# Performance work log

Hardware: AMD Instinct MI355X
Metric: run time of the kernel (lower is better)

The kernel has to match this reference:

```python
import jax, jax.numpy as jnp
import numpy as np

IN_DIM = 128
OUT_DIM = 128
NUM_RELS = 8
N_NODES = 50000
N_EDGES = 500000


def setup_inputs() -> dict:
    key = jax.random.key(0)
    k_x, k_ei_s, k_ei_d, k_et, k_w, k_sw = jax.random.split(key, 6)
    x = jax.random.normal(k_x, (N_NODES, IN_DIM), dtype=jnp.float32)
    src = jax.random.randint(k_ei_s, (N_EDGES,), 0, N_NODES)
    dst = jax.random.randint(k_ei_d, (N_EDGES,), 0, N_NODES)
    edge_index = jnp.stack([src, dst], axis=0).astype(jnp.int64)
    edge_type = jax.random.randint(k_et, (N_EDGES,), 0, NUM_RELS).astype(jnp.int64)
    # xavier_uniform: bound = sqrt(6/(fan_in+fan_out))
    bw = float(np.sqrt(6.0 / (IN_DIM + OUT_DIM)))
    weight = jax.random.uniform(k_w, (NUM_RELS, IN_DIM, OUT_DIM), dtype=jnp.float32, minval=-bw, maxval=bw)
    self_loop_weight = jax.random.uniform(k_sw, (IN_DIM, OUT_DIM), dtype=jnp.float32, minval=-bw, maxval=bw)
    bias = jnp.zeros((OUT_DIM,), dtype=jnp.float32)
    return {
        "x": x,
        "weight": weight,
        "self_loop_weight": self_loop_weight,
        "bias": bias,
        "edge_index": edge_index,
        "edge_type": edge_type,
        "num_entities": N_NODES,
    }


def reference(x, weight, self_loop_weight, bias, edge_index, edge_type, num_entities):
    # Relation-grouped formulation of the per-edge loop:
    # transform every node under every relation once: hr[r, n, o]
    hr = jnp.einsum("nd,rdo->rno", x, weight)
    src, dst = edge_index[0], edge_index[1]
    # per-edge message = x[src] @ weight[edge_type]  == hr[edge_type, src]
    msg = hr[edge_type, src]  # [E, out]
    agg = jax.ops.segment_sum(msg, dst, num_segments=num_entities)  # scatter-add into out[dst]
    out = agg + x @ self_loop_weight + bias
    return jax.nn.relu(out)
```

## Files before the change

### kernel.cpp

```cpp
#include <hip/hip_runtime.h>

#define IN_DIM 128
#define OUT_DIM 128
#define NUM_RELS 8
#define SCAN_ELEMS 2048

typedef unsigned short u16;
typedef u16 u16x8 __attribute__((ext_vector_type(8)));
typedef u16 u16x4 __attribute__((ext_vector_type(4)));
typedef __bf16 bf16x8 __attribute__((ext_vector_type(8)));
typedef float f32x4 __attribute__((ext_vector_type(4)));

__device__ __forceinline__ u16 f2bf(float f) {
    unsigned u = __float_as_uint(f);
    u += 0x7FFF + ((u >> 16) & 1);
    return (u16)(u >> 16);
}
__device__ __forceinline__ float bf2f(u16 h) {
    return __uint_as_float((unsigned)h << 16);
}

__global__ __launch_bounds__(256) void k_f2bf(
    const float* __restrict__ in, u16* __restrict__ out, long n)
{
    long i = ((long)blockIdx.x * blockDim.x + threadIdx.x) * 4;
    if (i >= n) return;
    float4 v = *(const float4*)(in + i);
    u16x4 o;
    o[0] = f2bf(v.x); o[1] = f2bf(v.y); o[2] = f2bf(v.z); o[3] = f2bf(v.w);
    *(u16x4*)(out + i) = o;
}

__global__ __launch_bounds__(256) void k_f2bf_w(
    const float* __restrict__ weight, const float* __restrict__ slw,
    u16* __restrict__ out)
{
    int i = (blockIdx.x * blockDim.x + threadIdx.x) * 4;
    if (i >= 9 * 16384) return;
    const float* src = (i < 8 * 16384) ? (weight + i) : (slw + (i - 8 * 16384));
    float4 v = *(const float4*)src;
    u16x4 o;
    o[0] = f2bf(v.x); o[1] = f2bf(v.y); o[2] = f2bf(v.z); o[3] = f2bf(v.w);
    *(u16x4*)(out + i) = o;
}

__global__ __launch_bounds__(256, 2) void mfma_gemm2(
    const u16* __restrict__ xb,
    const u16* __restrict__ Wb,
    const float* __restrict__ bias,
    u16* __restrict__ hr,
    int N, int ntiles)
{
    __shared__ u16 slab[4][16 * 68];

    const int tid   = threadIdx.x;
    const int z     = blockIdx.z;
    const int wv    = tid >> 6;
    const int lane  = tid & 63;
    const int q     = lane >> 4;
    const int l     = lane & 15;
    const int mbase = (wv >> 1) * 64;
    const int cbase = (wv & 1) * 64;

    const u16* Wz = Wb + (size_t)z * 128 * 128;

    u16x8 Bf[4][4];
    #pragma unroll
    for (int nt = 0; nt < 4; ++nt) {
        const int col = cbase + nt * 16 + l;
        #pragma unroll
        for (int kc = 0; kc < 4; ++kc) {
            const int k0 = kc * 32 + q * 8;
            #pragma unroll
            for (int j = 0; j < 8; ++j)
                Bf[nt][kc][j] = Wz[(k0 + j) * 128 + col];
        }
    }

    float bv[4];
    #pragma unroll
    for (int nt = 0; nt < 4; ++nt)
        bv[nt] = (z == 8) ? bias[cbase + nt * 16 + l] : 0.f;

    u16* slabw = &slab[wv][0];

    for (int tile = blockIdx.x; tile < ntiles; tile += gridDim.x) {
        const int n0 = tile * 128;

        f32x4 acc[4][4] = {};

        #pragma unroll
        for (int kc = 0; kc < 4; ++kc) {
            const int k0 = kc * 32 + q * 8;
            u16x8 a[4];
            #pragma unroll
            for (int mt = 0; mt < 4; ++mt) {
                const int row = n0 + mbase + mt * 16 + l;
                u16x8 v = {};
                if (row < N) v = *(const u16x8*)(xb + (size_t)row * 128 + k0);
                a[mt] = v;
            }
            #pragma unroll
            for (int nt = 0; nt < 4; ++nt) {
                bf16x8 b = __builtin_bit_cast(bf16x8, Bf[nt][kc]);
                #pragma unroll
                for (int mt = 0; mt < 4; ++mt) {
                    acc[mt][nt] = __builtin_amdgcn_mfma_f32_16x16x32_bf16(
                        __builtin_bit_cast(bf16x8, a[mt]), b, acc[mt][nt], 0, 0, 0);
                }
            }
        }

        u16* hrz = hr + ((size_t)z * N) * 128;
        #pragma unroll
        for (int mt = 0; mt < 4; ++mt) {
            #pragma unroll
            for (int nt = 0; nt < 4; ++nt) {
                const int col = nt * 16 + l;
                #pragma unroll
                for (int j = 0; j < 4; ++j) {
                    slabw[(q * 4 + j) * 68 + col] = f2bf(acc[mt][nt][j] + bv[nt]);
                }
            }
            const int srow = lane >> 3;
            const int scol = (lane & 7) * 8;
            #pragma unroll
            for (int h = 0; h < 2; ++h) {
                const int r = h * 8 + srow;
                const int grow = n0 + mbase + mt * 16 + r;
                if (grow < N) {
                    u16x8 v = *(const u16x8*)&slabw[r * 68 + scol];
                    *(u16x8*)(hrz + (size_t)grow * 128 + cbase + scol) = v;
                }
            }
        }
    }
}

__global__ __launch_bounds__(256) void k_zero(int* __restrict__ p, int n)
{
    int i = blockIdx.x * blockDim.x + threadIdx.x;
    if (i < n) p[i] = 0;
}

__global__ __launch_bounds__(256) void k_hist(
    const int* __restrict__ dst, int* __restrict__ deg, int E)
{
    int e = blockIdx.x * blockDim.x + threadIdx.x;
    if (e < E) atomicAdd(&deg[dst[e]], 1);
}

__global__ __launch_bounds__(256) void k_scan1(
    const int* __restrict__ deg, int* __restrict__ local,
    int* __restrict__ bsum, int n)
{
    __shared__ int s[256];
    const int t = threadIdx.x;
    const int base = blockIdx.x * SCAN_ELEMS + t * 8;
    int v[8];
    int sum = 0;
    #pragma unroll
    for (int j = 0; j < 8; ++j) {
        int i = base + j;
        v[j] = (i < n) ? deg[i] : 0;
        sum += v[j];
    }
    s[t] = sum;
    __syncthreads();
    #pragma unroll
    for (int off = 1; off < 256; off <<= 1) {
        int y = (t >= off) ? s[t - off] : 0;
        __syncthreads();
        s[t] += y;
        __syncthreads();
    }
    int run = s[t] - sum;
    #pragma unroll
    for (int j = 0; j < 8; ++j) {
        int i = base + j;
        if (i < n) local[i] = run;
        run += v[j];
    }
    if (t == 255) bsum[blockIdx.x] = s[255];
}

__global__ __launch_bounds__(256) void k_scan2(
    int* __restrict__ bsum, int* __restrict__ row_ptr, int B, int n)
{
    __shared__ int s[256];
    const int t = threadIdx.x;
    int v = (t < B) ? bsum[t] : 0;
    s[t] = v;
    __syncthreads();
    #pragma unroll
    for (int off = 1; off < 256; off <<= 1) {
        int y = (t >= off) ? s[t - off] : 0;
        __syncthreads();
        s[t] += y;
        __syncthreads();
    }
    if (t < B) bsum[t] = s[t] - v;
    if (t == 255) row_ptr[n] = s[255];
}

__global__ __launch_bounds__(256) void k_scan3(
    int* __restrict__ row_ptr, const int* __restrict__ bsum,
    int* __restrict__ cursor, int n)
{
    const int t = threadIdx.x;
    const int base = blockIdx.x * SCAN_ELEMS + t * 8;
    const int off = bsum[blockIdx.x];
    #pragma unroll
    for (int j = 0; j < 8; ++j) {
        int i = base + j;
        if (i < n) {
            int val = row_ptr[i] + off;
            row_ptr[i] = val;
            cursor[i] = val;
        }
    }
}

__global__ __launch_bounds__(256) void k_fill(
    const int* __restrict__ src, const int* __restrict__ dst,
    const int* __restrict__ et, int* __restrict__ cursor,
    int* __restrict__ packed, int E)
{
    int e = blockIdx.x * blockDim.x + threadIdx.x;
    if (e >= E) return;
    int pos = atomicAdd(&cursor[dst[e]], 1);
    packed[pos] = (et[e] << 17) | src[e];
}

__global__ __launch_bounds__(256) void gather_bf16(
    const u16* __restrict__ hr,
    const u16* __restrict__ hself,
    const int* __restrict__ row_ptr, const int* __restrict__ packed,
    float* __restrict__ out, int Nn, int N)
{
    int g = blockIdx.x * 8 + (threadIdx.x >> 5);
    int lane = threadIdx.x & 31;
    if (g >= Nn) return;
    const int beg = row_ptr[g];
    const int end = row_ptr[g + 1];

    u16x4 s = *(const u16x4*)(hself + (size_t)g * 128 + lane * 4);
    float a0 = bf2f(s[0]), a1 = bf2f(s[1]), a2 = bf2f(s[2]), a3 = bf2f(s[3]);

    for (int k = beg; k < end; ++k) {
        int p = packed[k];
        int sn = p & 0x1FFFF;
        int r  = p >> 17;
        u16x4 v = *(const u16x4*)(hr + ((size_t)r * N + sn) * 128 + lane * 4);
        a0 += bf2f(v[0]); a1 += bf2f(v[1]); a2 += bf2f(v[2]); a3 += bf2f(v[3]);
    }
    float4 o = make_float4(fmaxf(a0, 0.f), fmaxf(a1, 0.f),
                           fmaxf(a2, 0.f), fmaxf(a3, 0.f));
    *(float4*)(out + (size_t)g * 128 + lane * 4) = o;
}

__global__ __launch_bounds__(256) void gemm128(
    const float* __restrict__ x, const float* __restrict__ W,
    const float* __restrict__ bias, float* __restrict__ out, int N)
{
    __shared__ float Ws[IN_DIM * OUT_DIM];
    __shared__ float xs[16][IN_DIM];

    const float* Wz = W + (size_t)blockIdx.z * IN_DIM * OUT_DIM;
    float* outz = out + (size_t)blockIdx.z * (size_t)N * OUT_DIM;

    {
        const float4* s4 = (const float4*)Wz;
        float4* d4 = (float4*)Ws;
        for (int i = threadIdx.x; i < IN_DIM * OUT_DIM / 4; i += 256)
            d4[i] = s4[i];
    }

    const int tid = threadIdx.x;
    const int nl = (tid >> 5) * 2;
    const int og = (tid & 31) * 4;

    float4 b4 = make_float4(0.f, 0.f, 0.f, 0.f);
    if (bias) b4 = *(const float4*)&bias[og];

    const int nchunks = (N + 15) / 16;
    for (int chunk = blockIdx.x; chunk < nchunks; chunk += gridDim.x) {
        const int n0 = chunk * 16;
        const int rows = min(16, N - n0);
        __syncthreads();
        {
            const float4* xsrc = (const float4*)(x + (size_t)n0 * IN_DIM);
            float4* xdst = (float4*)&xs[0][0];
            const int n4 = rows * (IN_DIM / 4);
            for (int i = tid; i < n4; i += 256) xdst[i] = xsrc[i];
        }
        __syncthreads();

        if (nl < rows) {
            float a00 = 0.f, a01 = 0.f, a02 = 0.f, a03 = 0.f;
            float a10 = 0.f, a11 = 0.f, a12 = 0.f, a13 = 0.f;
            #pragma unroll 8
            for (int d = 0; d < IN_DIM; ++d) {
                const float4 w4 = *(const float4*)&Ws[d * OUT_DIM + og];
                const float xa = xs[nl][d];
                const float xb = xs[nl + 1][d];
                a00 += xa * w4.x; a01 += xa * w4.y; a02 += xa * w4.z; a03 += xa * w4.w;
                a10 += xb * w4.x; a11 += xb * w4.y; a12 += xb * w4.z; a13 += xb * w4.w;
            }
            float4 r0 = make_float4(a00 + b4.x, a01 + b4.y, a02 + b4.z, a03 + b4.w);
            *(float4*)&outz[(size_t)(n0 + nl) * OUT_DIM + og] = r0;
            if (nl + 1 < rows) {
                float4 r1 = make_float4(a10 + b4.x, a11 + b4.y, a12 + b4.z, a13 + b4.w);
                *(float4*)&outz[(size_t)(n0 + nl + 1) * OUT_DIM + og] = r1;
            }
        }
    }
}

__global__ __launch_bounds__(256) void edge_direct(
    const float* __restrict__ x, const float* __restrict__ W,
    const int* __restrict__ src, const int* __restrict__ dst,
    const int* __restrict__ et, float* __restrict__ out, int E)
{
    long t = (long)blockIdx.x * blockDim.x + threadIdx.x;
    long e = t >> 6;
    int lane = (int)(t & 63);
    if (e >= E) return;
    int s = src[e], d = dst[e], r = et[e];
    const float* xr = x + (long)s * IN_DIM;
    float2 xv = *(const float2*)(xr + lane * 2);
    const float* Wr = W + (long)r * IN_DIM * OUT_DIM;
    const int o0 = lane * 2;
    float a0 = 0.f, a1 = 0.f;
    #pragma unroll 8
    for (int dd = 0; dd < 64; ++dd) {
        float xa = __shfl(xv.x, dd);
        float xb = __shfl(xv.y, dd);
        a0 += xa * Wr[(2 * dd) * OUT_DIM + o0]     + xb * Wr[(2 * dd + 1) * OUT_DIM + o0];
        a1 += xa * Wr[(2 * dd) * OUT_DIM + o0 + 1] + xb * Wr[(2 * dd + 1) * OUT_DIM + o0 + 1];
    }
    atomicAdd(out + (long)d * OUT_DIM + o0, a0);
    atomicAdd(out + (long)d * OUT_DIM + o0 + 1, a1);
}

__global__ __launch_bounds__(256) void relu_k(float* __restrict__ out, long n4)
{
    long i = (long)blockIdx.x * blockDim.x + threadIdx.x;
    if (i >= n4) return;
    float4 v = ((float4*)out)[i];
    v.x = fmaxf(v.x, 0.f); v.y = fmaxf(v.y, 0.f);
    v.z = fmaxf(v.z, 0.f); v.w = fmaxf(v.w, 0.f);
    ((float4*)out)[i] = v;
}

static inline size_t align256(size_t x) { return (x + 255) & ~(size_t)255; }

extern "C" void kernel_launch(void* const* d_in, const int* in_sizes, int n_in,
                              void* d_out, int out_size, void* d_ws, size_t ws_size,
                              hipStream_t stream)
{
    const float* x      = (const float*)d_in[0];
    const float* weight = (const float*)d_in[1];
    const float* slw    = (const float*)d_in[2];
    const float* bias   = (const float*)d_in[3];
    const int*   ei     = (const int*)d_in[4];
    const int*   et     = (const int*)d_in[5];

    const int N = in_sizes[0] / IN_DIM;
    const int E = in_sizes[5];
    const int* src  = ei;
    const int* dstp = ei + E;

    float* out = (float*)d_out;

    size_t off = 0;
    const size_t xb_off   = off; off += align256((size_t)N * 128 * 2);
    const size_t wb_off   = off; off += align256((size_t)9 * 128 * 128 * 2);
    const size_t hr_off   = off; off += align256((size_t)9 * N * 128 * 2);
    const size_t rp_off   = off; off += align256((size_t)(N + 1) * 4);
    const size_t cur_off  = off; off += align256((size_t)N * 4);
    const size_t pk_off   = off; off += align256((size_t)E * 4);
    const size_t bs_off   = off; off += align256(256 * 4);
    const size_t need_bf16 = off;

    const int scanB = (N + SCAN_ELEMS - 1) / SCAN_ELEMS;

    if (ws_size >= need_bf16 && N <= (1 << 17) && scanB <= 256) {
        char* base   = (char*)d_ws;
        u16* xb      = (u16*)(base + xb_off);
        u16* Wbq     = (u16*)(base + wb_off);
        u16* hr      = (u16*)(base + hr_off);
        int* row_ptr = (int*)(base + rp_off);
        int* cursor  = (int*)(base + cur_off);
        int* packed  = (int*)(base + pk_off);
        int* bsum    = (int*)(base + bs_off);

        long nx = (long)N * 128;
        k_f2bf<<<dim3((nx / 4 + 255) / 256), 256, 0, stream>>>(x, xb, nx);
        k_f2bf_w<<<dim3((9 * 16384 / 4 + 255) / 256), 256, 0, stream>>>(weight, slw, Wbq);

        k_zero<<<dim3((N + 255) / 256), 256, 0, stream>>>(cursor, N);
        k_hist<<<dim3((E + 255) / 256), 256, 0, stream>>>(dstp, cursor, E);
        k_scan1<<<dim3(scanB), 256, 0, stream>>>(cursor, row_ptr, bsum, N);
        k_scan2<<<dim3(1), 256, 0, stream>>>(bsum, row_ptr, scanB, N);
        k_scan3<<<dim3(scanB), 256, 0, stream>>>(row_ptr, bsum, cursor, N);
        k_fill<<<dim3((E + 255) / 256), 256, 0, stream>>>(src, dstp, et, cursor, packed, E);

        const int ntiles = (N + 127) / 128;
        mfma_gemm2<<<dim3(56, 1, 9), 256, 0, stream>>>(xb, Wbq, bias, hr, N, ntiles);

        gather_bf16<<<dim3((N + 7) / 8), 256, 0, stream>>>(
            hr, hr + (size_t)8 * N * 128, row_ptr, packed, out, N, N);
    } else if (ws_size >= (size_t)NUM_RELS * N * 128 * 4) {
        gemm128<<<dim3(512, 1, 1), 256, 0, stream>>>(x, slw, bias, out, N);
        long nt = (long)E * 64;
        edge_direct<<<dim3((nt + 255) / 256), 256, 0, stream>>>(x, weight, src, dstp, et, out, E);
        long n4 = (long)N * OUT_DIM / 4;
        relu_k<<<dim3((n4 + 255) / 256), 256, 0, stream>>>(out, n4);
    } else {
        gemm128<<<dim3(512, 1, 1), 256, 0, stream>>>(x, slw, bias, out, N);
        long nt = (long)E * 64;
        edge_direct<<<dim3((nt + 255) / 256), 256, 0, stream>>>(x, weight, src, dstp, et, out, E);
        long n4 = (long)N * OUT_DIM / 4;
        relu_k<<<dim3((n4 + 255) / 256), 256, 0, stream>>>(out, n4);
    }
}
```

Before: 225.7 us.

## Fuse prep kernels, transpose weights, one-tile-per-block GEMM, unroll gather by four

Merges the x conversion, weight conversion and cursor zeroing into one prep kernel, cutting two launches. Weights are stored transposed so the GEMM loads B fragments as vector loads instead of scalar strided gathers. The GEMM drops its persistent tile loop and launches one block per tile, and the gather loop is unrolled by four with independent accumulators to put more loads in flight. The costs are more GEMM blocks, each reloading its B fragments, and scattered 2-byte stores in the weight transpose.

```diff
diff --git a/kernel.cpp b/kernel.cpp
--- a/kernel.cpp
+++ b/kernel.cpp
@@ -20,36 +20,48 @@
     return __uint_as_float((unsigned)h << 16);
 }
 
-__global__ __launch_bounds__(256) void k_f2bf(
-    const float* __restrict__ in, u16* __restrict__ out, long n)
-{
-    long i = ((long)blockIdx.x * blockDim.x + threadIdx.x) * 4;
-    if (i >= n) return;
-    float4 v = *(const float4*)(in + i);
-    u16x4 o;
-    o[0] = f2bf(v.x); o[1] = f2bf(v.y); o[2] = f2bf(v.z); o[3] = f2bf(v.w);
-    *(u16x4*)(out + i) = o;
-}
-
-__global__ __launch_bounds__(256) void k_f2bf_w(
-    const float* __restrict__ weight, const float* __restrict__ slw,
-    u16* __restrict__ out)
-{
-    int i = (blockIdx.x * blockDim.x + threadIdx.x) * 4;
-    if (i >= 9 * 16384) return;
-    const float* src = (i < 8 * 16384) ? (weight + i) : (slw + (i - 8 * 16384));
-    float4 v = *(const float4*)src;
-    u16x4 o;
-    o[0] = f2bf(v.x); o[1] = f2bf(v.y); o[2] = f2bf(v.z); o[3] = f2bf(v.w);
-    *(u16x4*)(out + i) = o;
-}
-
-__global__ __launch_bounds__(256, 2) void mfma_gemm2(
+__global__ __launch_bounds__(256) void k_prep(
+    const float* __restrict__ x, const float* __restrict__ weight,
+    const float* __restrict__ slw,
+    u16* __restrict__ xb, u16* __restrict__ WbT, int* __restrict__ cursor,
+    int N, int BA, int BB)
+{
+    const int b = blockIdx.x;
+    const int tid = threadIdx.x;
+    if (b < BA) {
+        long i = ((long)b * 256 + tid) * 4;
+        if (i < (long)N * 128) {
+            float4 v = *(const float4*)(x + i);
+            u16x4 o;
+            o[0] = f2bf(v.x); o[1] = f2bf(v.y); o[2] = f2bf(v.z); o[3] = f2bf(v.w);
+            *(u16x4*)(xb + i) = o;
+        }
+    } else if (b < BA + BB) {
+        int t = (b - BA) * 256 + tid;
+        int z = t >> 12;
+        int rem = t & 4095;
+        int kk = rem >> 5;
+        int c0 = (rem & 31) * 4;
+        const float* srcp = (z < 8) ? (weight + (size_t)z * 16384 + kk * 128 + c0)
+                                    : (slw + kk * 128 + c0);
+        float4 v = *(const float4*)srcp;
+        u16* outz = WbT + (size_t)z * 16384;
+        outz[(c0 + 0) * 128 + kk] = f2bf(v.x);
+        outz[(c0 + 1) * 128 + kk] = f2bf(v.y);
+        outz[(c0 + 2) * 128 + kk] = f2bf(v.z);
+        outz[(c0 + 3) * 128 + kk] = f2bf(v.w);
+    } else {
+        int j = (b - BA - BB) * 256 + tid;
+        if (j < N) cursor[j] = 0;
+    }
+}
+
+__global__ __launch_bounds__(256, 2) void mfma_gemm3(
     const u16* __restrict__ xb,
-    const u16* __restrict__ Wb,
+    const u16* __restrict__ WbT,
     const float* __restrict__ bias,
     u16* __restrict__ hr,
-    int N, int ntiles)
+    int N)
 {
     __shared__ u16 slab[4][16 * 68];
 
@@ -61,20 +73,17 @@
     const int l     = lane & 15;
     const int mbase = (wv >> 1) * 64;
     const int cbase = (wv & 1) * 64;
-
-    const u16* Wz = Wb + (size_t)z * 128 * 128;
+    const int n0    = blockIdx.x * 128;
+
+    const u16* Wz = WbT + (size_t)z * 16384;
 
     u16x8 Bf[4][4];
     #pragma unroll
     for (int nt = 0; nt < 4; ++nt) {
-        const int col = cbase + nt * 16 + l;
+        const u16* colp = Wz + (cbase + nt * 16 + l) * 128;
         #pragma unroll
-        for (int kc = 0; kc < 4; ++kc) {
-            const int k0 = kc * 32 + q * 8;
-            #pragma unroll
-            for (int j = 0; j < 8; ++j)
-                Bf[nt][kc][j] = Wz[(k0 + j) * 128 + col];
-        }
+        for (int kc = 0; kc < 4; ++kc)
+            Bf[nt][kc] = *(const u16x8*)(colp + kc * 32 + q * 8);
     }
 
     float bv[4];
@@ -82,65 +91,52 @@
     for (int nt = 0; nt < 4; ++nt)
         bv[nt] = (z == 8) ? bias[cbase + nt * 16 + l] : 0.f;
 
-    u16* slabw = &slab[wv][0];
-
-    for (int tile = blockIdx.x; tile < ntiles; tile += gridDim.x) {
-        const int n0 = tile * 128;
-
-        f32x4 acc[4][4] = {};
-
+    f32x4 acc[4][4] = {};
+    #pragma unroll
+    for (int kc = 0; kc < 4; ++kc) {
+        const int k0 = kc * 32 + q * 8;
+        u16x8 a[4];
         #pragma unroll
-        for (int kc = 0; kc < 4; ++kc) {
-            const int k0 = kc * 32 + q * 8;
-            u16x8 a[4];
+        for (int mt = 0; mt < 4; ++mt) {
+            const int row = n0 + mbase + mt * 16 + l;
+            u16x8 v = {};
+            if (row < N) v = *(const u16x8*)(xb + (size_t)row * 128 + k0);
+            a[mt] = v;
+        }
+        #pragma unroll
+        for (int nt = 0; nt < 4; ++nt) {
+            bf16x8 b = __builtin_bit_cast(bf16x8, Bf[nt][kc]);
             #pragma unroll
             for (int mt = 0; mt < 4; ++mt) {
-                const int row = n0 + mbase + mt * 16 + l;
-                u16x8 v = {};
-                if (row < N) v = *(const u16x8*)(xb + (size_t)row * 128 + k0);
-                a[mt] = v;
+                acc[mt][nt] = __builtin_amdgcn_mfma_f32_16x16x32_bf16(
+                    __builtin_bit_cast(bf16x8, a[mt]), b, acc[mt][nt], 0, 0, 0);
             }
+        }
+    }
+
+    u16* slabw = &slab[wv][0];
+    u16* hrz = hr + ((size_t)z * N) * 128;
+    #pragma unroll
+    for (int mt = 0; mt < 4; ++mt) {
+        #pragma unroll
+        for (int nt = 0; nt < 4; ++nt) {
+            const int col = nt * 16 + l;
             #pragma unroll
-            for (int nt = 0; nt < 4; ++nt) {
-                bf16x8 b = __builtin_bit_cast(bf16x8, Bf[nt][kc]);
-                #pragma unroll
-                for (int mt = 0; mt < 4; ++mt) {
-                    acc[mt][nt] = __builtin_amdgcn_mfma_f32_16x16x32_bf16(
-                        __builtin_bit_cast(bf16x8, a[mt]), b, acc[mt][nt], 0, 0, 0);
-                }
+            for (int j = 0; j < 4; ++j)
+                slabw[(q * 4 + j) * 68 + col] = f2bf(acc[mt][nt][j] + bv[nt]);
+        }
+        const int srow = lane >> 3;
+        const int scol = (lane & 7) * 8;
+        #pragma unroll
+        for (int h = 0; h < 2; ++h) {
+            const int r = h * 8 + srow;
+            const int grow = n0 + mbase + mt * 16 + r;
+            if (grow < N) {
+                u16x8 v = *(const u16x8*)&slabw[r * 68 + scol];
+                *(u16x8*)(hrz + (size_t)grow * 128 + cbase + scol) = v;
             }
         }
-
-        u16* hrz = hr + ((size_t)z * N) * 128;
-        #pragma unroll
-        for (int mt = 0; mt < 4; ++mt) {
-            #pragma unroll
-            for (int nt = 0; nt < 4; ++nt) {
-                const int col = nt * 16 + l;
-                #pragma unroll
-                for (int j = 0; j < 4; ++j) {
-                    slabw[(q * 4 + j) * 68 + col] = f2bf(acc[mt][nt][j] + bv[nt]);
-                }
-            }
-            const int srow = lane >> 3;
-            const int scol = (lane & 7) * 8;
-            #pragma unroll
-            for (int h = 0; h < 2; ++h) {
-                const int r = h * 8 + srow;
-                const int grow = n0 + mbase + mt * 16 + r;
-                if (grow < N) {
-                    u16x8 v = *(const u16x8*)&slabw[r * 68 + scol];
-                    *(u16x8*)(hrz + (size_t)grow * 128 + cbase + scol) = v;
-                }
-            }
-        }
-    }
-}
-
-__global__ __launch_bounds__(256) void k_zero(int* __restrict__ p, int n)
-{
-    int i = blockIdx.x * blockDim.x + threadIdx.x;
-    if (i < n) p[i] = 0;
+    }
 }
 
 __global__ __launch_bounds__(256) void k_hist(
@@ -246,14 +242,31 @@
 
     u16x4 s = *(const u16x4*)(hself + (size_t)g * 128 + lane * 4);
     float a0 = bf2f(s[0]), a1 = bf2f(s[1]), a2 = bf2f(s[2]), a3 = bf2f(s[3]);
-
-    for (int k = beg; k < end; ++k) {
+    float b0 = 0.f, b1 = 0.f, b2 = 0.f, b3 = 0.f;
+    float c0 = 0.f, c1 = 0.f, c2 = 0.f, c3 = 0.f;
+    float d0 = 0.f, d1 = 0.f, d2 = 0.f, d3 = 0.f;
+
+    const int lo = lane * 4;
+    int k = beg;
+    for (; k + 4 <= end; k += 4) {
+        int p0 = packed[k], p1 = packed[k + 1], p2 = packed[k + 2], p3 = packed[k + 3];
+        u16x4 v0 = *(const u16x4*)(hr + ((size_t)(p0 >> 17) * N + (p0 & 0x1FFFF)) * 128 + lo);
+        u16x4 v1 = *(const u16x4*)(hr + ((size_t)(p1 >> 17) * N + (p1 & 0x1FFFF)) * 128 + lo);
+        u16x4 v2 = *(const u16x4*)(hr + ((size_t)(p2 >> 17) * N + (p2 & 0x1FFFF)) * 128 + lo);
+        u16x4 v3 = *(const u16x4*)(hr + ((size_t)(p3 >> 17) * N + (p3 & 0x1FFFF)) * 128 + lo);
+        a0 += bf2f(v0[0]); a1 += bf2f(v0[1]); a2 += bf2f(v0[2]); a3 += bf2f(v0[3]);
+        b0 += bf2f(v1[0]); b1 += bf2f(v1[1]); b2 += bf2f(v1[2]); b3 += bf2f(v1[3]);
+        c0 += bf2f(v2[0]); c1 += bf2f(v2[1]); c2 += bf2f(v2[2]); c3 += bf2f(v2[3]);
+        d0 += bf2f(v3[0]); d1 += bf2f(v3[1]); d2 += bf2f(v3[2]); d3 += bf2f(v3[3]);
+    }
+    for (; k < end; ++k) {
         int p = packed[k];
-        int sn = p & 0x1FFFF;
-        int r  = p >> 17;
-        u16x4 v = *(const u16x4*)(hr + ((size_t)r * N + sn) * 128 + lane * 4);
+        u16x4 v = *(const u16x4*)(hr + ((size_t)(p >> 17) * N + (p & 0x1FFFF)) * 128 + lo);
         a0 += bf2f(v[0]); a1 += bf2f(v[1]); a2 += bf2f(v[2]); a3 += bf2f(v[3]);
     }
+    a0 += b0 + c0 + d0; a1 += b1 + c1 + d1;
+    a2 += b2 + c2 + d2; a3 += b3 + c3 + d3;
+
     float4 o = make_float4(fmaxf(a0, 0.f), fmaxf(a1, 0.f),
                            fmaxf(a2, 0.f), fmaxf(a3, 0.f));
     *(float4*)(out + (size_t)g * 128 + lane * 4) = o;
@@ -388,18 +401,19 @@
     if (ws_size >= need_bf16 && N <= (1 << 17) && scanB <= 256) {
         char* base   = (char*)d_ws;
         u16* xb      = (u16*)(base + xb_off);
-        u16* Wbq     = (u16*)(base + wb_off);
+        u16* WbT     = (u16*)(base + wb_off);
         u16* hr      = (u16*)(base + hr_off);
         int* row_ptr = (int*)(base + rp_off);
         int* cursor  = (int*)(base + cur_off);
         int* packed  = (int*)(base + pk_off);
         int* bsum    = (int*)(base + bs_off);
 
-        long nx = (long)N * 128;
-        k_f2bf<<<dim3((nx / 4 + 255) / 256), 256, 0, stream>>>(x, xb, nx);
-        k_f2bf_w<<<dim3((9 * 16384 / 4 + 255) / 256), 256, 0, stream>>>(weight, slw, Wbq);
-
-        k_zero<<<dim3((N + 255) / 256), 256, 0, stream>>>(cursor, N);
+        const int BA = (int)(((long)N * 128 / 4 + 255) / 256);
+        const int BB = 9 * 4096 / 256;
+        const int BC = (N + 255) / 256;
+        k_prep<<<dim3(BA + BB + BC), 256, 0, stream>>>(
+            x, weight, slw, xb, WbT, cursor, N, BA, BB);
+
         k_hist<<<dim3((E + 255) / 256), 256, 0, stream>>>(dstp, cursor, E);
         k_scan1<<<dim3(scanB), 256, 0, stream>>>(cursor, row_ptr, bsum, N);
         k_scan2<<<dim3(1), 256, 0, stream>>>(bsum, row_ptr, scanB, N);
@@ -407,7 +421,7 @@
         k_fill<<<dim3((E + 255) / 256), 256, 0, stream>>>(src, dstp, et, cursor, packed, E);
 
         const int ntiles = (N + 127) / 128;
-        mfma_gemm2<<<dim3(56, 1, 9), 256, 0, stream>>>(xb, Wbq, bias, hr, N, ntiles);
+        mfma_gemm3<<<dim3(ntiles, 1, 9), 256, 0, stream>>>(xb, WbT, bias, hr, N);
 
         gather_bf16<<<dim3((N + 7) / 8), 256, 0, stream>>>(
             hr, hr + (size_t)8 * N * 128, row_ptr, packed, out, N, N);
```

After: 235.4 us. +4.3%, slower.
